# Kernel tuning notes

Measured on AMD Instinct MI355X. Metric: run time of the kernel, lower is better.

The kernel has to match this reference:

```python
import jax, jax.numpy as jnp
import numpy as np

D_MODEL = 1024
NUM_HEADS = 16
D_K = D_MODEL // NUM_HEADS
SCALE = float(np.sqrt(D_K))


def setup_inputs() -> dict:
    key = jax.random.key(0)
    ks = jax.random.split(key, 9)
    B, S = 4, 2048
    x = jax.random.normal(ks[0], (B, S, D_MODEL), dtype=jnp.float32)
    init = 1.0 / np.sqrt(D_MODEL)
    def lin(kw, kb):
        W = jax.random.uniform(kw, (D_MODEL, D_MODEL), jnp.float32, -init, init)
        b = jax.random.uniform(kb, (D_MODEL,), jnp.float32, -init, init)
        return W, b
    Wq, bq = lin(ks[1], ks[2])
    Wk, bk = lin(ks[3], ks[4])
    Wv, bv = lin(ks[5], ks[6])
    Wo, bo = lin(ks[7], ks[8])
    return {"x": x, "Wq": Wq, "bq": bq, "Wk": Wk, "bk": bk,
            "Wv": Wv, "bv": bv, "Wo": Wo, "bo": bo}


def reference(x, Wq, bq, Wk, bk, Wv, bv, Wo, bo):
    B, S, _ = x.shape
    # projections (torch Linear: y = x @ W.T + b)
    q = x @ Wq.T + bq
    k = x @ Wk.T + bk
    v = x @ Wv.T + bv
    # [B, H, S, d_k]
    q = q.reshape(B, S, NUM_HEADS, D_K).transpose(0, 2, 1, 3)
    k = k.reshape(B, S, NUM_HEADS, D_K).transpose(0, 2, 1, 3)
    v = v.reshape(B, S, NUM_HEADS, D_K).transpose(0, 2, 1, 3)
    # explicit scores [B, H, S, S]
    scores = jnp.einsum('bhqd,bhkd->bhqk', q, k) / SCALE
    attn = jax.nn.softmax(scores, axis=-1)
    # dropout is identity in eval mode
    ctx = jnp.einsum('bhqk,bhkd->bhqd', attn, v)
    ctx = ctx.transpose(0, 2, 1, 3).reshape(B, S, D_MODEL)
    return ctx @ Wo.T + bo
```

## Files before the change

kernel.cpp:

```cpp
#include <hip/hip_runtime.h>
#include <stdint.h>


typedef __attribute__((ext_vector_type(8))) short short8;
typedef __attribute__((ext_vector_type(4))) float f32x4;
typedef __attribute__((ext_vector_type(16))) float f32x16;
typedef __attribute__((ext_vector_type(4))) unsigned int u32x4;
typedef __attribute__((ext_vector_type(4))) unsigned short us4;
typedef unsigned short ushort_t;
typedef unsigned int uint_t;

#define DMODEL 1024
#define SEQ 2048
#define NH 16
#define QSCALE 0.18033688011112043f

__device__ __forceinline__ ushort_t bfbits(float f) {
  uint32_t u = __float_as_uint(f);
  u = (u + 0x7fffu + ((u >> 16) & 1u)) >> 16;
  return (ushort_t)u;
}
__device__ __forceinline__ uint_t cvt_pk_bf16(float lo, float hi) {
  uint_t r;
  asm("v_cvt_pk_bf16_f32 %0, %1, %2" : "=v"(r) : "v"(lo), "v"(hi));
  return r;
}
__device__ __forceinline__ float exp2_hw(float x) {
  float r;
  asm("v_exp_f32 %0, %1" : "=v"(r) : "v"(x));
  return r;
}
__device__ __forceinline__ f32x16 mfma32(short8 a, short8 b, f32x16 c) {
  return __builtin_amdgcn_mfma_f32_32x32x16_bf16(a, b, c, 0, 0, 0);
}

typedef __attribute__((address_space(1))) void gvoid_t;
typedef __attribute__((address_space(3))) void lvoid_t;
__device__ __forceinline__ void gl_lds16(const void* gp, void* lp) {
  __builtin_amdgcn_global_load_lds((gvoid_t*)(uintptr_t)gp, (lvoid_t*)lp, 16, 0, 0);
}

__global__ __launch_bounds__(256) void cvt_bf16(const float* __restrict__ in,
                                                ushort_t* __restrict__ out) {
  int i = (int)(blockIdx.x * 256u + threadIdx.x) * 8;
  const float4* p = (const float4*)(in + i);
  float4 a = p[0], b = p[1];
  short8 o;
  o[0] = (short)bfbits(a.x); o[1] = (short)bfbits(a.y);
  o[2] = (short)bfbits(a.z); o[3] = (short)bfbits(a.w);
  o[4] = (short)bfbits(b.x); o[5] = (short)bfbits(b.y);
  o[6] = (short)bfbits(b.z); o[7] = (short)bfbits(b.w);
  *(short8*)(out + i) = o;
}

__global__ __launch_bounds__(256) void cvt4_bf16(const float* __restrict__ w0,
                                                 const float* __restrict__ w1,
                                                 const float* __restrict__ w2,
                                                 const float* __restrict__ w3,
                                                 ushort_t* __restrict__ out) {
  int which = (int)(blockIdx.x >> 9);
  const float* src = (which == 0) ? w0 : (which == 1) ? w1 : (which == 2) ? w2 : w3;
  int i = (int)(((blockIdx.x & 511) * 256u) + threadIdx.x) * 8;
  const float4* p = (const float4*)(src + i);
  float4 a = p[0], b = p[1];
  short8 o;
  o[0] = (short)bfbits(a.x); o[1] = (short)bfbits(a.y);
  o[2] = (short)bfbits(a.z); o[3] = (short)bfbits(a.w);
  o[4] = (short)bfbits(b.x); o[5] = (short)bfbits(b.y);
  o[6] = (short)bfbits(b.z); o[7] = (short)bfbits(b.w);
  *(short8*)(out + (size_t)which * 1048576 + i) = o;
}

#define EPI_QKV 0
#define EPI_OUT 1

template <int EPI>
__global__ __launch_bounds__(256) void gemm_bt(const ushort_t* __restrict__ A,
                                               const ushort_t* __restrict__ Bw,
                                               const float* __restrict__ b0,
                                               const float* __restrict__ b1,
                                               const float* __restrict__ b2,
                                               ushort_t* __restrict__ Qb,
                                               ushort_t* __restrict__ Kb,
                                               ushort_t* __restrict__ Vtb,
                                               float* __restrict__ Yf) {
  __shared__ alignas(16) ushort_t As[3][128 * 32];
  __shared__ alignas(16) ushort_t Bs[3][128 * 32];
  const int tid = threadIdx.x;
  const int lane = tid & 63, w = tid >> 6;
  const int g = lane >> 4, r16 = lane & 15;
  const int wr = w >> 1, wc = w & 1;

  int flat = (int)(blockIdx.x + gridDim.x * blockIdx.y);
  int xcd = flat & 7, local = flat >> 3;
  int bm0, bn0;
  if (EPI == EPI_QKV) {
    bm0 = ((xcd & 3) * 16 + (local & 15)) * 128;
    bn0 = ((xcd >> 2) * 12 + (local >> 4)) * 128;
  } else {
    bm0 = (xcd * 8 + (local & 7)) * 128;
    bn0 = (local >> 3) * 128;
  }

  f32x4 acc[4][4];
#pragma unroll
  for (int m = 0; m < 4; ++m)
#pragma unroll
    for (int n = 0; n < 4; ++n) acc[m][n] = (f32x4){0.f, 0.f, 0.f, 0.f};

  const int srow = tid >> 2;
  const int scs = ((tid & 3) ^ ((tid >> 3) & 3)) * 8;
  const int rsw = (r16 >> 1) & 3;

  auto stage = [&](int bf, int k0) {
    char* AsB = (char*)As[bf];
    char* BsB = (char*)Bs[bf];
    gl_lds16(A + (size_t)(bm0 + srow) * DMODEL + k0 + scs, AsB + w * 1024);
    gl_lds16(A + (size_t)(bm0 + 64 + srow) * DMODEL + k0 + scs, AsB + w * 1024 + 4096);
    gl_lds16(Bw + (size_t)(bn0 + srow) * DMODEL + k0 + scs, BsB + w * 1024);
    gl_lds16(Bw + (size_t)(bn0 + 64 + srow) * DMODEL + k0 + scs, BsB + w * 1024 + 4096);
  };

  stage(0, 0);
  stage(1, 32);
  int buf = 0;
  for (int t = 0; t < 32; ++t) {
    if (t < 31)
      asm volatile("s_waitcnt vmcnt(4)\n\ts_barrier" ::: "memory");
    else
      asm volatile("s_waitcnt vmcnt(0)\n\ts_barrier" ::: "memory");
    if (t < 30) stage((t + 2) % 3, (t + 2) * 32);

    const char* AsB = (const char*)As[buf];
    const char* BsB = (const char*)Bs[buf];
    short8 af[4], bfr[4];
#pragma unroll
    for (int m = 0; m < 4; ++m)
      af[m] = *(const short8*)(AsB + (wr * 64 + m * 16 + r16) * 64 + (g ^ rsw) * 16);
#pragma unroll
    for (int n = 0; n < 4; ++n)
      bfr[n] = *(const short8*)(BsB + (wc * 64 + n * 16 + r16) * 64 + (g ^ rsw) * 16);
    __builtin_amdgcn_s_setprio(1);
#pragma unroll
    for (int m = 0; m < 4; ++m)
#pragma unroll
      for (int n = 0; n < 4; ++n)
        acc[m][n] = __builtin_amdgcn_mfma_f32_16x16x32_bf16(af[m], bfr[n], acc[m][n], 0, 0, 0);
    __builtin_amdgcn_s_setprio(0);
    buf = (buf == 2) ? 0 : buf + 1;
  }

  if (EPI == EPI_OUT) {
    float bv[4];
#pragma unroll
    for (int n = 0; n < 4; ++n) bv[n] = b0[bn0 + wc * 64 + n * 16 + r16];
#pragma unroll
    for (int m = 0; m < 4; ++m)
#pragma unroll
      for (int r = 0; r < 4; ++r) {
        int grow = bm0 + wr * 64 + m * 16 + 4 * g + r;
        float* orow = Yf + (size_t)grow * DMODEL + bn0 + wc * 64;
#pragma unroll
        for (int n = 0; n < 4; ++n) orow[n * 16 + r16] = acc[m][n][r] + bv[n];
      }
  } else {
    int mat = bn0 >> 10;
    const float* bias = (mat == 0) ? b0 : (mat == 1 ? b1 : b2);
    ushort_t* dQK = (mat == 0) ? Qb : Kb;
    int nc0 = bn0 & 1023;
    float scl = (mat == 0) ? QSCALE : 1.0f;
    float bv[4];
#pragma unroll
    for (int n = 0; n < 4; ++n) bv[n] = bias[nc0 + wc * 64 + n * 16 + r16];
    if (mat < 2) {
#pragma unroll
      for (int m = 0; m < 4; ++m)
#pragma unroll
        for (int r = 0; r < 4; ++r) {
          int grow = bm0 + wr * 64 + m * 16 + 4 * g + r;
          int b = grow >> 11, s = grow & 2047;
#pragma unroll
          for (int n = 0; n < 4; ++n) {
            int gcl = nc0 + wc * 64 + n * 16 + r16;
            int h = gcl >> 6, d = gcl & 63;
            dQK[((size_t)(b * NH + h) * SEQ + s) * 64 + d] = bfbits((acc[m][n][r] + bv[n]) * scl);
          }
        }
    } else {
#pragma unroll
      for (int m = 0; m < 4; ++m) {
        int grow0 = bm0 + wr * 64 + m * 16 + 4 * g;
        int b = grow0 >> 11, s0 = grow0 & 2047;
#pragma unroll
        for (int n = 0; n < 4; ++n) {
          int gcl = nc0 + wc * 64 + n * 16 + r16;
          int h = gcl >> 6, d = gcl & 63;
          us4 pk;
          pk[0] = bfbits(acc[m][n][0] + bv[n]);
          pk[1] = bfbits(acc[m][n][1] + bv[n]);
          pk[2] = bfbits(acc[m][n][2] + bv[n]);
          pk[3] = bfbits(acc[m][n][3] + bv[n]);
          *(us4*)(Vtb + ((size_t)(b * NH + h) * 64 + d) * SEQ + s0) = pk;
        }
      }
    }
  }
}

__global__ __launch_bounds__(512, 4) void attn_fwd(const ushort_t* __restrict__ Q,
                                                   const ushort_t* __restrict__ K,
                                                   const ushort_t* __restrict__ Vt,
                                                   ushort_t* __restrict__ ctx) {
  __shared__ alignas(16) ushort_t Ks[3][64 * 64];
  __shared__ alignas(16) ushort_t Vs[3][64 * 64];
  const int tid = threadIdx.x;
  const int lane = tid & 63, w = tid >> 6;
  const int q32 = lane & 31, h = lane >> 5;

  int flat = (int)(blockIdx.x + 8 * blockIdx.y);
  int sw = (flat & 7) * 64 + (flat >> 3);
  int bh = sw >> 3, q0 = (sw & 7) * 256;

  const ushort_t* Qp = Q + (size_t)bh * SEQ * 64;
  const ushort_t* Kp = K + (size_t)bh * SEQ * 64;
  const ushort_t* Vp = Vt + (size_t)bh * 64 * SEQ;

  short8 qf[4];
  {
    const ushort_t* qr = Qp + (size_t)(q0 + w * 32 + q32) * 64 + h * 8;
    qf[0] = *(const short8*)(qr);
    qf[1] = *(const short8*)(qr + 16);
    qf[2] = *(const short8*)(qr + 32);
    qf[3] = *(const short8*)(qr + 48);
  }

  f32x16 o0 = (f32x16)0.0f, o1 = (f32x16)0.0f;
  float l = 0.f;

  const int swz = (q32 & 7) << 4;

  auto stage = [&](int bf, int kv0) {
    int row = tid >> 3;
    int cs = (tid & 7) ^ (row & 7);
    gl_lds16(Kp + (size_t)(kv0 + row) * 64 + cs * 8, (char*)Ks[bf] + w * 1024);
    gl_lds16(Vp + (size_t)row * SEQ + kv0 + cs * 8, (char*)Vs[bf] + w * 1024);
  };

  stage(0, 0);
  stage(1, 64);
  int buf = 0;
  for (int t = 0; t < 32; ++t) {
    if (t < 31)
      asm volatile("s_waitcnt vmcnt(2)\n\ts_barrier" ::: "memory");
    else
      asm volatile("s_waitcnt vmcnt(0)\n\ts_barrier" ::: "memory");
    if (t < 30) stage((t + 2) % 3, (t + 2) * 64);

    const char* kb0 = (const char*)Ks[buf] + q32 * 128;
    const char* kb1 = kb0 + 32 * 128;
    const char* vb0 = (const char*)Vs[buf] + q32 * 128;
    const char* vb1 = vb0 + 32 * 128;

    f32x16 s0 = (f32x16)0.0f, s1 = (f32x16)0.0f;
    __builtin_amdgcn_s_setprio(1);
#pragma unroll
    for (int c = 0; c < 4; ++c) {
      short8 kf0 = *(const short8*)(kb0 + ((32 * c + 16 * h) ^ swz));
      short8 kf1 = *(const short8*)(kb1 + ((32 * c + 16 * h) ^ swz));
      s0 = mfma32(kf0, qf[c], s0);
      s1 = mfma32(kf1, qf[c], s1);
    }
    __builtin_amdgcn_s_setprio(0);

#pragma unroll
    for (int j = 0; j < 16; ++j) {
      s0[j] = exp2_hw(s0[j]);
      s1[j] = exp2_hw(s1[j]);
    }

    {
      f32x16 ts = s0 + s1;
      float a = (ts[0] + ts[1]) + (ts[2] + ts[3]);
      float b = (ts[4] + ts[5]) + (ts[6] + ts[7]);
      float c2 = (ts[8] + ts[9]) + (ts[10] + ts[11]);
      float d = (ts[12] + ts[13]) + (ts[14] + ts[15]);
      l += (a + b) + (c2 + d);
    }

    uint_t pw[16];
#pragma unroll
    for (int i = 0; i < 8; ++i) {
      pw[i] = cvt_pk_bf16(s0[2 * i], s0[2 * i + 1]);
      pw[8 + i] = cvt_pk_bf16(s1[2 * i], s1[2 * i + 1]);
    }
#pragma unroll
    for (int c = 0; c < 4; ++c) {
      asm volatile("v_permlane32_swap_b32 %0, %1" : "+v"(pw[4 * c]), "+v"(pw[4 * c + 2]));
      asm volatile("v_permlane32_swap_b32 %0, %1" : "+v"(pw[4 * c + 1]), "+v"(pw[4 * c + 3]));
    }

    __builtin_amdgcn_s_setprio(1);
#pragma unroll
    for (int c = 0; c < 4; ++c) {
      u32x4 pk = {pw[4 * c], pw[4 * c + 1], pw[4 * c + 2], pw[4 * c + 3]};
      short8 pfc = __builtin_bit_cast(short8, pk);
      short8 vf0 = *(const short8*)(vb0 + ((32 * c + 16 * h) ^ swz));
      short8 vf1 = *(const short8*)(vb1 + ((32 * c + 16 * h) ^ swz));
      o0 = mfma32(vf0, pfc, o0);
      o1 = mfma32(vf1, pfc, o1);
    }
    __builtin_amdgcn_s_setprio(0);

    buf = (buf == 2) ? 0 : buf + 1;
  }

  float ltot = l + __shfl_xor(l, 32);
  float inv = 1.0f / ltot;
  int b = bh >> 4, hd = bh & 15;
  uint_t* crow = (uint_t*)(ctx + ((size_t)(b * SEQ + q0 + w * 32 + q32)) * DMODEL + hd * 64);
#pragma unroll
  for (int i = 0; i < 8; ++i) {
    int ui = (i & 1) + 4 * (i >> 1) + 2 * h;
    crow[ui] = cvt_pk_bf16(o0[2 * i] * inv, o0[2 * i + 1] * inv);
    crow[16 + ui] = cvt_pk_bf16(o1[2 * i] * inv, o1[2 * i + 1] * inv);
  }
}

extern "C" void kernel_launch(void* const* d_in, const int* in_sizes, int n_in,
                              void* d_out, int out_size, void* d_ws, size_t ws_size,
                              hipStream_t stream) {
  (void)in_sizes; (void)n_in; (void)out_size; (void)ws_size;
  const float* x  = (const float*)d_in[0];
  const float* Wq = (const float*)d_in[1];
  const float* bq = (const float*)d_in[2];
  const float* Wk = (const float*)d_in[3];
  const float* bk = (const float*)d_in[4];
  const float* Wv = (const float*)d_in[5];
  const float* bv = (const float*)d_in[6];
  const float* Wo = (const float*)d_in[7];
  const float* bo = (const float*)d_in[8];
  float* out = (float*)d_out;

  ushort_t* xb  = (ushort_t*)d_ws;
  ushort_t* w3  = xb + 8388608;
  ushort_t* wob = w3 + 3145728;
  ushort_t* Qb  = wob + 1048576;
  ushort_t* Kb  = Qb + 8388608;
  ushort_t* Vtb = Kb + 8388608;
  ushort_t* cx  = Vtb + 8388608;

  cvt_bf16<<<4096, 256, 0, stream>>>(x, xb);
  cvt4_bf16<<<2048, 256, 0, stream>>>(Wq, Wk, Wv, Wo, w3);

  gemm_bt<EPI_QKV><<<dim3(64, 24), 256, 0, stream>>>(xb, w3, bq, bk, bv, Qb, Kb, Vtb, nullptr);
  attn_fwd<<<dim3(8, 64), 512, 0, stream>>>(Qb, Kb, Vtb, cx);
  gemm_bt<EPI_OUT><<<dim3(64, 8), 256, 0, stream>>>(cx, wob, bo, nullptr, nullptr,
                                                    nullptr, nullptr, nullptr, out);
}
```

Baseline: 273.1 us.

## Load K/V fragments directly from global memory, dropping LDS staging in attention

The attention kernel no longer stages K and V tiles into shared memory through a triple-buffered async copy with barriers. Each wave now loads its own K and V MFMA fragments straight from global memory into registers, prefetching the next 32-key step one iteration ahead. Blocks shrink to 256 threads covering 128 queries, so the grid grows to 1024 blocks. This removes LDS traffic and block-wide barriers, but every wave re-reads the same K/V rows from global/L2 memory rather than sharing one staged copy, and each iteration now does half as much MFMA work per global load round-trip.

New measurement: 425.6 us. +55.9%, slower.

```diff
diff --git a/kernel.cpp b/kernel.cpp
--- a/kernel.cpp
+++ b/kernel.cpp
@@ -207,23 +207,21 @@
   }
 }
 
-__global__ __launch_bounds__(512, 4) void attn_fwd(const ushort_t* __restrict__ Q,
+__global__ __launch_bounds__(256, 4) void attn_fwd(const ushort_t* __restrict__ Q,
                                                    const ushort_t* __restrict__ K,
                                                    const ushort_t* __restrict__ Vt,
                                                    ushort_t* __restrict__ ctx) {
-  __shared__ alignas(16) ushort_t Ks[3][64 * 64];
-  __shared__ alignas(16) ushort_t Vs[3][64 * 64];
   const int tid = threadIdx.x;
   const int lane = tid & 63, w = tid >> 6;
   const int q32 = lane & 31, h = lane >> 5;
 
-  int flat = (int)(blockIdx.x + 8 * blockIdx.y);
-  int sw = (flat & 7) * 64 + (flat >> 3);
-  int bh = sw >> 3, q0 = (sw & 7) * 256;
+  int flat = (int)blockIdx.x;
+  int sw = (flat & 7) * 128 + (flat >> 3);
+  int bh = sw >> 4, q0 = (sw & 15) * 128;
 
   const ushort_t* Qp = Q + (size_t)bh * SEQ * 64;
-  const ushort_t* Kp = K + (size_t)bh * SEQ * 64;
-  const ushort_t* Vp = Vt + (size_t)bh * 64 * SEQ;
+  const ushort_t* Kp = K + (size_t)bh * SEQ * 64 + (size_t)q32 * 64 + 8 * h;
+  const ushort_t* Vp = Vt + (size_t)bh * 64 * SEQ + (size_t)q32 * SEQ + 8 * h;
 
   short8 qf[4];
   {
@@ -237,81 +235,60 @@
   f32x16 o0 = (f32x16)0.0f, o1 = (f32x16)0.0f;
   float l = 0.f;
 
-  const int swz = (q32 & 7) << 4;
-
-  auto stage = [&](int bf, int kv0) {
-    int row = tid >> 3;
-    int cs = (tid & 7) ^ (row & 7);
-    gl_lds16(Kp + (size_t)(kv0 + row) * 64 + cs * 8, (char*)Ks[bf] + w * 1024);
-    gl_lds16(Vp + (size_t)row * SEQ + kv0 + cs * 8, (char*)Vs[bf] + w * 1024);
+  short8 kf[4], vf[2][2];
+  auto loadK = [&](int kv0) {
+#pragma unroll
+    for (int c = 0; c < 4; ++c)
+      kf[c] = *(const short8*)(Kp + (size_t)kv0 * 64 + 16 * c);
   };
-
-  stage(0, 0);
-  stage(1, 64);
-  int buf = 0;
-  for (int t = 0; t < 32; ++t) {
-    if (t < 31)
-      asm volatile("s_waitcnt vmcnt(2)\n\ts_barrier" ::: "memory");
-    else
-      asm volatile("s_waitcnt vmcnt(0)\n\ts_barrier" ::: "memory");
-    if (t < 30) stage((t + 2) % 3, (t + 2) * 64);
-
-    const char* kb0 = (const char*)Ks[buf] + q32 * 128;
-    const char* kb1 = kb0 + 32 * 128;
-    const char* vb0 = (const char*)Vs[buf] + q32 * 128;
-    const char* vb1 = vb0 + 32 * 128;
-
-    f32x16 s0 = (f32x16)0.0f, s1 = (f32x16)0.0f;
+  auto loadV = [&](int kv0) {
+#pragma unroll
+    for (int db = 0; db < 2; ++db)
+#pragma unroll
+      for (int c2 = 0; c2 < 2; ++c2)
+        vf[db][c2] = *(const short8*)(Vp + (size_t)db * 32 * SEQ + kv0 + 16 * c2);
+  };
+
+  loadK(0);
+  loadV(0);
+#pragma unroll 1
+  for (int t = 0; t < 64; ++t) {
+    f32x16 s = (f32x16)0.0f;
     __builtin_amdgcn_s_setprio(1);
 #pragma unroll
-    for (int c = 0; c < 4; ++c) {
-      short8 kf0 = *(const short8*)(kb0 + ((32 * c + 16 * h) ^ swz));
-      short8 kf1 = *(const short8*)(kb1 + ((32 * c + 16 * h) ^ swz));
-      s0 = mfma32(kf0, qf[c], s0);
-      s1 = mfma32(kf1, qf[c], s1);
-    }
+    for (int c = 0; c < 4; ++c) s = mfma32(kf[c], qf[c], s);
     __builtin_amdgcn_s_setprio(0);
-
-#pragma unroll
-    for (int j = 0; j < 16; ++j) {
-      s0[j] = exp2_hw(s0[j]);
-      s1[j] = exp2_hw(s1[j]);
-    }
-
+    if (t < 63) loadK((t + 1) * 32);
+
+#pragma unroll
+    for (int j = 0; j < 16; ++j) s[j] = exp2_hw(s[j]);
     {
-      f32x16 ts = s0 + s1;
-      float a = (ts[0] + ts[1]) + (ts[2] + ts[3]);
-      float b = (ts[4] + ts[5]) + (ts[6] + ts[7]);
-      float c2 = (ts[8] + ts[9]) + (ts[10] + ts[11]);
-      float d = (ts[12] + ts[13]) + (ts[14] + ts[15]);
+      float a = (s[0] + s[1]) + (s[2] + s[3]);
+      float b = (s[4] + s[5]) + (s[6] + s[7]);
+      float c2 = (s[8] + s[9]) + (s[10] + s[11]);
+      float d = (s[12] + s[13]) + (s[14] + s[15]);
       l += (a + b) + (c2 + d);
     }
 
-    uint_t pw[16];
-#pragma unroll
-    for (int i = 0; i < 8; ++i) {
-      pw[i] = cvt_pk_bf16(s0[2 * i], s0[2 * i + 1]);
-      pw[8 + i] = cvt_pk_bf16(s1[2 * i], s1[2 * i + 1]);
-    }
-#pragma unroll
-    for (int c = 0; c < 4; ++c) {
+    uint_t pw[8];
+#pragma unroll
+    for (int i = 0; i < 8; ++i) pw[i] = cvt_pk_bf16(s[2 * i], s[2 * i + 1]);
+#pragma unroll
+    for (int c = 0; c < 2; ++c) {
       asm volatile("v_permlane32_swap_b32 %0, %1" : "+v"(pw[4 * c]), "+v"(pw[4 * c + 2]));
       asm volatile("v_permlane32_swap_b32 %0, %1" : "+v"(pw[4 * c + 1]), "+v"(pw[4 * c + 3]));
     }
 
     __builtin_amdgcn_s_setprio(1);
 #pragma unroll
-    for (int c = 0; c < 4; ++c) {
-      u32x4 pk = {pw[4 * c], pw[4 * c + 1], pw[4 * c + 2], pw[4 * c + 3]};
+    for (int c2 = 0; c2 < 2; ++c2) {
+      u32x4 pk = {pw[4 * c2], pw[4 * c2 + 1], pw[4 * c2 + 2], pw[4 * c2 + 3]};
       short8 pfc = __builtin_bit_cast(short8, pk);
-      short8 vf0 = *(const short8*)(vb0 + ((32 * c + 16 * h) ^ swz));
-      short8 vf1 = *(const short8*)(vb1 + ((32 * c + 16 * h) ^ swz));
-      o0 = mfma32(vf0, pfc, o0);
-      o1 = mfma32(vf1, pfc, o1);
+      o0 = mfma32(vf[0][c2], pfc, o0);
+      o1 = mfma32(vf[1][c2], pfc, o1);
     }
     __builtin_amdgcn_s_setprio(0);
-
-    buf = (buf == 2) ? 0 : buf + 1;
+    if (t < 63) loadV((t + 1) * 32);
   }
 
   float ltot = l + __shfl_xor(l, 32);
@@ -353,7 +330,7 @@
   cvt4_bf16<<<2048, 256, 0, stream>>>(Wq, Wk, Wv, Wo, w3);
 
   gemm_bt<EPI_QKV><<<dim3(64, 24), 256, 0, stream>>>(xb, w3, bq, bk, bv, Qb, Kb, Vtb, nullptr);
-  attn_fwd<<<dim3(8, 64), 512, 0, stream>>>(Qb, Kb, Vtb, cx);
+  attn_fwd<<<1024, 256, 0, stream>>>(Qb, Kb, Vtb, cx);
   gemm_bt<EPI_OUT><<<dim3(64, 8), 256, 0, stream>>>(cx, wob, bo, nullptr, nullptr,
                                                     nullptr, nullptr, nullptr, out);
 }
```
